# Performance work log

Measured on AMD Instinct MI355X. Metric: run time of the kernel, lower is better.

Reference implementation:

```python
import jax, jax.numpy as jnp
import numpy as np
import math

PHI = (1 + math.sqrt(5)) / 2
ALPHA = 1 / PHI          # residual scale
BETA = 1 / PHI ** 2      # sparse-matmul scale
DIM = 1910
NZ = int(DIM * DIM / PHI)


def setup_inputs() -> dict:
    key = jax.random.key(0)
    kx, ki, kv = jax.random.split(key, 3)
    x = jax.random.normal(kx, (8, 4096, DIM), dtype=jnp.float32)
    W_indices = jax.random.randint(ki, (2, NZ), 0, DIM, dtype=jnp.int32)
    W_values = jax.random.normal(kv, (NZ,), dtype=jnp.float32) / math.sqrt(DIM)
    return {"x": x, "W_indices": W_indices, "W_values": W_values}


def reference(x, W_indices, W_values):
    dim = x.shape[-1]
    # COO -> dense: duplicate (row,col) entries sum, matching torch.sparse semantics.
    W = jnp.zeros((dim, dim), dtype=x.dtype).at[W_indices[0], W_indices[1]].add(W_values)
    orig_shape = x.shape
    xf = x.reshape(-1, dim)          # [tokens, dim]
    Wx = xf @ W.T                    # (W @ x.T).T == x @ W.T
    out = ALPHA * xf + BETA * Wx
    return out.reshape(orig_shape)
```

## Files before the change

### kernel.cpp

```cpp
#include <hip/hip_runtime.h>
#include <hip/hip_bf16.h>
#include <stdint.h>

#define DIMV 1910
#define KP   1920
#define NT   60
#define PHI_F  1.6180339887498949f
#define BETA_F 0.3819660112501051f

typedef __attribute__((ext_vector_type(4))) float f32x4;
typedef __attribute__((ext_vector_type(8))) short bf16x8;
typedef __attribute__((ext_vector_type(8))) unsigned short u16x8;

__device__ __forceinline__ void gl16(const void* g, void* l) {
    __builtin_amdgcn_global_load_lds(
        (const __attribute__((address_space(1))) void*)(uintptr_t)g,
        (__attribute__((address_space(3))) void*)(uint32_t)(uintptr_t)l,
        16, 0, 0);
}

__global__ void k_scatter(const int* __restrict__ ridx, const int* __restrict__ cidx,
                          const float* __restrict__ vals, float* __restrict__ Wd, int nz) {
    int i = blockIdx.x * 256 + threadIdx.x;
    if (i < nz) atomicAdd(Wd + (long)ridx[i] * DIMV + cidx[i], vals[i]);
}

__global__ void k_build_w(const float* __restrict__ Wd, unsigned short* __restrict__ Wb, int total8) {
    int stride = gridDim.x * blockDim.x;
    for (int i = blockIdx.x * blockDim.x + threadIdx.x; i < total8; i += stride) {
        int v = i * 8;
        int n = v / KP;
        int k = v - n * KP;
        u16x8 o;
#pragma unroll
        for (int j = 0; j < 8; ++j) {
            int kk = k + j;
            float fv = (n < DIMV && kk < DIMV) ? Wd[(size_t)n * DIMV + kk] : 0.f;
            if (kk == n && n < DIMV) fv += PHI_F;
            __hip_bfloat16 b = __float2bfloat16(fv);
            o[j] = *reinterpret_cast<unsigned short*>(&b);
        }
        *(u16x8*)(Wb + (size_t)v) = o;
    }
}

__global__ void k_conv_x(const float* __restrict__ x, unsigned short* __restrict__ xb, int total8) {
    int stride = gridDim.x * blockDim.x;
    for (int i = blockIdx.x * blockDim.x + threadIdx.x; i < total8; i += stride) {
        int v = i * 8;
        int row = v / KP;
        int col = v - row * KP;
        u16x8 o;
        if (col + 8 <= DIMV) {
            const float2* s = (const float2*)(x + (size_t)row * DIMV + col);
            float2 f0 = s[0], f1 = s[1], f2 = s[2], f3 = s[3];
            float f[8] = {f0.x, f0.y, f1.x, f1.y, f2.x, f2.y, f3.x, f3.y};
#pragma unroll
            for (int j = 0; j < 8; ++j) {
                __hip_bfloat16 b = __float2bfloat16(f[j]);
                o[j] = *reinterpret_cast<unsigned short*>(&b);
            }
        } else {
#pragma unroll
            for (int j = 0; j < 8; ++j) {
                int c = col + j;
                float fv = (c < DIMV) ? x[(size_t)row * DIMV + c] : 0.f;
                __hip_bfloat16 b = __float2bfloat16(fv);
                o[j] = *reinterpret_cast<unsigned short*>(&b);
            }
        }
        *(u16x8*)(xb + (size_t)v) = o;
    }
}

__global__ __launch_bounds__(512, 2) void k_gemm(const short* __restrict__ A,
                                                 const short* __restrict__ B,
                                                 float* __restrict__ C) {
    __shared__ short As[3 * 256 * 32];
    __shared__ short Bs[3 * 256 * 32];

    const int bid = blockIdx.x;
    const int bn  = bid & 7;
    const int bm  = bid >> 3;

    const int tid = threadIdx.x;
    const int w   = tid >> 6;
    const int l   = tid & 63;
    const int wm  = w >> 2;
    const int wn  = w & 3;
    const int fr  = l & 15;
    const int q   = l >> 4;

    const int srow  = tid >> 2;
    const int lslot = (tid & 3) ^ ((tid >> 3) & 3);
    const char* aG = (const char*)A + ((size_t)(bm * 256 + srow) * KP) * 2 + lslot * 16;
    const char* bG = (const char*)B + ((size_t)(bn * 256 + srow) * KP) * 2 + lslot * 16;
    const size_t gstep = (size_t)128 * KP * 2;
    char* aL0 = (char*)As + tid * 16;
    char* bL0 = (char*)Bs + tid * 16;

    const int co    = (q ^ ((fr >> 1) & 3)) * 16;
    const int aBase = (wm * 128 + fr) * 64 + co;
    const int bBase = (wn * 64  + fr) * 64 + co;

    f32x4 acc[8][4] = {};

#pragma unroll
    for (int tt = 0; tt < 2; ++tt) {
        const char* ga = aG + tt * 64;
        const char* gb = bG + tt * 64;
        char* la = aL0 + tt * 16384;
        char* lb = bL0 + tt * 16384;
        gl16(ga, la); gl16(ga + gstep, la + 8192);
        gl16(gb, lb); gl16(gb + gstep, lb + 8192);
    }
    asm volatile("s_waitcnt vmcnt(4)" ::: "memory");
    __builtin_amdgcn_s_barrier();
    asm volatile("" ::: "memory");

    int rdo = 0;
    int sto = 2 * 16384;

#pragma unroll 3
    for (int t = 0; t < NT; ++t) {
        const char* pa = (const char*)As + rdo + aBase;
        const char* pb = (const char*)Bs + rdo + bBase;

        bf16x8 af[8], b01[2];
#pragma unroll
        for (int mi = 0; mi < 8; ++mi) af[mi] = *(const bf16x8*)(pa + mi * 1024);
#pragma unroll
        for (int ni = 0; ni < 2; ++ni) b01[ni] = *(const bf16x8*)(pb + ni * 1024);
        if (t + 2 < NT) {
            const char* g = aG + (size_t)(t + 2) * 64;
            gl16(g, aL0 + sto); gl16(g + gstep, aL0 + sto + 8192);
        }
        asm volatile("" ::: "memory");
        __builtin_amdgcn_s_barrier();
        asm volatile("" ::: "memory");
        __builtin_amdgcn_s_setprio(1);
#pragma unroll
        for (int mi = 0; mi < 8; ++mi)
#pragma unroll
            for (int ni = 0; ni < 2; ++ni)
                acc[mi][ni] = __builtin_amdgcn_mfma_f32_16x16x32_bf16(af[mi], b01[ni], acc[mi][ni], 0, 0, 0);
        __builtin_amdgcn_s_setprio(0);
        asm volatile("" ::: "memory");
        __builtin_amdgcn_s_barrier();
        asm volatile("" ::: "memory");

        bf16x8 b23[2];
#pragma unroll
        for (int ni = 0; ni < 2; ++ni) b23[ni] = *(const bf16x8*)(pb + (ni + 2) * 1024);
        if (t + 2 < NT) {
            const char* g = bG + (size_t)(t + 2) * 64;
            gl16(g, bL0 + sto); gl16(g + gstep, bL0 + sto + 8192);
            asm volatile("s_waitcnt vmcnt(4)" ::: "memory");
        } else {
            asm volatile("s_waitcnt vmcnt(0)" ::: "memory");
        }
        __builtin_amdgcn_s_barrier();
        asm volatile("" ::: "memory");
        __builtin_amdgcn_s_setprio(1);
#pragma unroll
        for (int mi = 0; mi < 8; ++mi)
#pragma unroll
            for (int ni = 0; ni < 2; ++ni)
                acc[mi][ni + 2] = __builtin_amdgcn_mfma_f32_16x16x32_bf16(af[mi], b23[ni], acc[mi][ni + 2], 0, 0, 0);
        __builtin_amdgcn_s_setprio(0);
        asm volatile("" ::: "memory");
        __builtin_amdgcn_s_barrier();
        asm volatile("" ::: "memory");

        rdo += 16384; if (rdo == 49152) rdo = 0;
        sto += 16384; if (sto == 49152) sto = 0;
    }

    const int grow0 = bm * 256 + wm * 128 + q * 4;
    const int gcol0 = bn * 256 + wn * 64 + fr;
#pragma unroll
    for (int mi = 0; mi < 8; ++mi) {
#pragma unroll
        for (int ni = 0; ni < 4; ++ni) {
            int gcol = gcol0 + ni * 16;
            if (gcol < DIMV) {
                size_t base = (size_t)(grow0 + mi * 16) * DIMV + gcol;
#pragma unroll
                for (int r = 0; r < 4; ++r)
                    C[base + (size_t)r * DIMV] = BETA_F * acc[mi][ni][r];
            }
        }
    }
}

extern "C" void kernel_launch(void* const* d_in, const int* in_sizes, int n_in,
                              void* d_out, int out_size, void* d_ws, size_t ws_size,
                              hipStream_t stream) {
    const float* x    = (const float*)d_in[0];
    const int*   widx = (const int*)d_in[1];
    const float* wval = (const float*)d_in[2];
    float* out = (float*)d_out;

    const int nz = in_sizes[2];
    const int M  = in_sizes[0] / DIMV;

    const size_t xb_bytes = (size_t)M * KP * 2;
    const size_t wb_bytes = (size_t)2048 * KP * 2;
    const size_t wd_bytes = (size_t)DIMV * DIMV * 4;
    char* ws = (char*)d_ws;
    unsigned short* xb = (unsigned short*)ws;
    unsigned short* Wb = (unsigned short*)(ws + xb_bytes);
    float*          Wd = (float*)ws;
    if (ws_size < xb_bytes + wb_bytes) return;
    (void)wd_bytes;

    hipMemsetAsync(Wd, 0, wd_bytes, stream);
    k_scatter<<<(nz + 255) / 256, 256, 0, stream>>>(widx, widx + nz, wval, Wd, nz);
    k_build_w<<<1800, 256, 0, stream>>>(Wd, Wb, KP * KP / 8);
    k_conv_x<<<2048, 256, 0, stream>>>(x, xb, M * KP / 8);
    k_gemm<<<1024, 512, 0, stream>>>((const short*)xb, (const short*)Wb, out);
}
```

Before: 477.2 us.

## Restructure GEMM main loop to K=64 double-buffered tiles with four-phase MFMA schedule

The GEMM K-step grows from 32 to 64, which halves the number of main-loop iterations. The LDS layout changes from a triple buffer of 32-wide tiles to a double buffer of 64-wide tiles (128 KB), using a new XOR swizzle over 8 slots. Each iteration is split into four quadrant phases so LDS fragment loads, global-to-LDS staging and MFMA blocks interleave across barriers. The intent is fewer barriers and less loop overhead per FLOP. The cost is that prefetch depth drops from two stages ahead to one, and the larger LDS footprint may limit occupancy to the declared two blocks per CU.

```diff
diff --git a/kernel.cpp b/kernel.cpp
--- a/kernel.cpp
+++ b/kernel.cpp
@@ -4,7 +4,7 @@
 
 #define DIMV 1910
 #define KP   1920
-#define NT   60
+#define NT   30
 #define PHI_F  1.6180339887498949f
 #define BETA_F 0.3819660112501051f
 
@@ -76,8 +76,7 @@
 __global__ __launch_bounds__(512, 2) void k_gemm(const short* __restrict__ A,
                                                  const short* __restrict__ B,
                                                  float* __restrict__ C) {
-    __shared__ short As[3 * 256 * 32];
-    __shared__ short Bs[3 * 256 * 32];
+    __shared__ char lds[131072];
 
     const int bid = blockIdx.x;
     const int bn  = bid & 7;
@@ -91,90 +90,138 @@
     const int fr  = l & 15;
     const int q   = l >> 4;
 
-    const int srow  = tid >> 2;
-    const int lslot = (tid & 3) ^ ((tid >> 3) & 3);
-    const char* aG = (const char*)A + ((size_t)(bm * 256 + srow) * KP) * 2 + lslot * 16;
-    const char* bG = (const char*)B + ((size_t)(bn * 256 + srow) * KP) * 2 + lslot * 16;
-    const size_t gstep = (size_t)128 * KP * 2;
-    char* aL0 = (char*)As + tid * 16;
-    char* bL0 = (char*)Bs + tid * 16;
-
-    const int co    = (q ^ ((fr >> 1) & 3)) * 16;
-    const int aBase = (wm * 128 + fr) * 64 + co;
-    const int bBase = (wn * 64  + fr) * 64 + co;
+    const int    rs   = tid >> 3;
+    const size_t KPB  = (size_t)KP * 2;
+    const char*  aSrc = (const char*)A + (size_t)(bm * 256 + rs) * KPB + (((tid & 7) ^ (rs & 7)) * 16);
+    const char*  bSrc = (const char*)B + (size_t)(bn * 256 + rs) * KPB + (((tid & 7) ^ (rs & 7)) * 16);
+    char* stDst = lds + tid * 16;
+
+    const int co0  = ((q    ) ^ (fr & 7)) * 16;
+    const int co1  = ((4 + q) ^ (fr & 7)) * 16;
+    const int aOff = (wm * 128 + fr) * 128;
+    const int bOff = 32768 + (wn * 64 + fr) * 128;
 
     f32x4 acc[8][4] = {};
 
-#pragma unroll
-    for (int tt = 0; tt < 2; ++tt) {
-        const char* ga = aG + tt * 64;
-        const char* gb = bG + tt * 64;
-        char* la = aL0 + tt * 16384;
-        char* lb = bL0 + tt * 16384;
-        gl16(ga, la); gl16(ga + gstep, la + 8192);
-        gl16(gb, lb); gl16(gb + gstep, lb + 8192);
-    }
-    asm volatile("s_waitcnt vmcnt(4)" ::: "memory");
+#define STAGE_A(tt, bo, s) gl16(aSrc + (size_t)(s) * 64 * KPB + (size_t)(tt) * 128, stDst + (bo) + (s) * 8192)
+#define STAGE_B(tt, bo, s) gl16(bSrc + (size_t)(s) * 64 * KPB + (size_t)(tt) * 128, stDst + (bo) + 32768 + (s) * 8192)
+
+#pragma unroll
+    for (int s = 0; s < 4; ++s) STAGE_A(0, 0, s);
+#pragma unroll
+    for (int s = 0; s < 4; ++s) STAGE_B(0, 0, s);
+    asm volatile("s_waitcnt vmcnt(0)" ::: "memory");
     __builtin_amdgcn_s_barrier();
     asm volatile("" ::: "memory");
 
-    int rdo = 0;
-    int sto = 2 * 16384;
-
-#pragma unroll 3
+    int bo = 0;
     for (int t = 0; t < NT; ++t) {
-        const char* pa = (const char*)As + rdo + aBase;
-        const char* pb = (const char*)Bs + rdo + bBase;
-
-        bf16x8 af[8], b01[2];
-#pragma unroll
-        for (int mi = 0; mi < 8; ++mi) af[mi] = *(const bf16x8*)(pa + mi * 1024);
-#pragma unroll
-        for (int ni = 0; ni < 2; ++ni) b01[ni] = *(const bf16x8*)(pb + ni * 1024);
-        if (t + 2 < NT) {
-            const char* g = aG + (size_t)(t + 2) * 64;
-            gl16(g, aL0 + sto); gl16(g + gstep, aL0 + sto + 8192);
-        }
-        asm volatile("" ::: "memory");
-        __builtin_amdgcn_s_barrier();
-        asm volatile("" ::: "memory");
-        __builtin_amdgcn_s_setprio(1);
-#pragma unroll
-        for (int mi = 0; mi < 8; ++mi)
-#pragma unroll
-            for (int ni = 0; ni < 2; ++ni)
-                acc[mi][ni] = __builtin_amdgcn_mfma_f32_16x16x32_bf16(af[mi], b01[ni], acc[mi][ni], 0, 0, 0);
-        __builtin_amdgcn_s_setprio(0);
-        asm volatile("" ::: "memory");
-        __builtin_amdgcn_s_barrier();
-        asm volatile("" ::: "memory");
-
-        bf16x8 b23[2];
-#pragma unroll
-        for (int ni = 0; ni < 2; ++ni) b23[ni] = *(const bf16x8*)(pb + (ni + 2) * 1024);
-        if (t + 2 < NT) {
-            const char* g = bG + (size_t)(t + 2) * 64;
-            gl16(g, bL0 + sto); gl16(g + gstep, bL0 + sto + 8192);
-            asm volatile("s_waitcnt vmcnt(4)" ::: "memory");
-        } else {
-            asm volatile("s_waitcnt vmcnt(0)" ::: "memory");
-        }
-        __builtin_amdgcn_s_barrier();
-        asm volatile("" ::: "memory");
-        __builtin_amdgcn_s_setprio(1);
-#pragma unroll
-        for (int mi = 0; mi < 8; ++mi)
-#pragma unroll
-            for (int ni = 0; ni < 2; ++ni)
-                acc[mi][ni + 2] = __builtin_amdgcn_mfma_f32_16x16x32_bf16(af[mi], b23[ni], acc[mi][ni + 2], 0, 0, 0);
-        __builtin_amdgcn_s_setprio(0);
-        asm volatile("" ::: "memory");
-        __builtin_amdgcn_s_barrier();
-        asm volatile("" ::: "memory");
-
-        rdo += 16384; if (rdo == 49152) rdo = 0;
-        sto += 16384; if (sto == 49152) sto = 0;
-    }
+        const int nbo = bo ^ 65536;
+        const char* pa = lds + bo + aOff;
+        const char* pb = lds + bo + bOff;
+        const bool st = (t + 1 < NT);
+        bf16x8 a[4][2], b[2][2];
+
+#pragma unroll
+        for (int mi = 0; mi < 4; ++mi) {
+            a[mi][0] = *(const bf16x8*)(pa + mi * 2048 + co0);
+            a[mi][1] = *(const bf16x8*)(pa + mi * 2048 + co1);
+        }
+#pragma unroll
+        for (int ni = 0; ni < 2; ++ni) {
+            b[ni][0] = *(const bf16x8*)(pb + ni * 2048 + co0);
+            b[ni][1] = *(const bf16x8*)(pb + ni * 2048 + co1);
+        }
+        if (st) { STAGE_A(t + 1, nbo, 0); STAGE_A(t + 1, nbo, 1); STAGE_A(t + 1, nbo, 2); }
+        asm volatile("s_waitcnt lgkmcnt(8)" ::: "memory");
+        __builtin_amdgcn_s_barrier();
+        asm volatile("s_waitcnt lgkmcnt(0)" ::: "memory");
+        __builtin_amdgcn_sched_barrier(0);
+        __builtin_amdgcn_s_setprio(1);
+#pragma unroll
+        for (int kk = 0; kk < 2; ++kk)
+#pragma unroll
+            for (int mi = 0; mi < 4; ++mi)
+#pragma unroll
+                for (int ni = 0; ni < 2; ++ni)
+                    acc[mi][ni] = __builtin_amdgcn_mfma_f32_16x16x32_bf16(a[mi][kk], b[ni][kk], acc[mi][ni], 0, 0, 0);
+        __builtin_amdgcn_s_setprio(0);
+        asm volatile("" ::: "memory");
+        __builtin_amdgcn_s_barrier();
+        asm volatile("" ::: "memory");
+
+#pragma unroll
+        for (int ni = 0; ni < 2; ++ni) {
+            b[ni][0] = *(const bf16x8*)(pb + 4096 + ni * 2048 + co0);
+            b[ni][1] = *(const bf16x8*)(pb + 4096 + ni * 2048 + co1);
+        }
+        if (st) { STAGE_A(t + 1, nbo, 3); STAGE_B(t + 1, nbo, 0); STAGE_B(t + 1, nbo, 1); }
+        asm volatile("" ::: "memory");
+        __builtin_amdgcn_s_barrier();
+        asm volatile("s_waitcnt lgkmcnt(0)" ::: "memory");
+        __builtin_amdgcn_sched_barrier(0);
+        __builtin_amdgcn_s_setprio(1);
+#pragma unroll
+        for (int kk = 0; kk < 2; ++kk)
+#pragma unroll
+            for (int mi = 0; mi < 4; ++mi)
+#pragma unroll
+                for (int ni = 0; ni < 2; ++ni)
+                    acc[mi][ni + 2] = __builtin_amdgcn_mfma_f32_16x16x32_bf16(a[mi][kk], b[ni][kk], acc[mi][ni + 2], 0, 0, 0);
+        __builtin_amdgcn_s_setprio(0);
+        asm volatile("" ::: "memory");
+        __builtin_amdgcn_s_barrier();
+        asm volatile("" ::: "memory");
+
+#pragma unroll
+        for (int mi = 0; mi < 4; ++mi) {
+            a[mi][0] = *(const bf16x8*)(pa + 8192 + mi * 2048 + co0);
+            a[mi][1] = *(const bf16x8*)(pa + 8192 + mi * 2048 + co1);
+        }
+        if (st) { STAGE_B(t + 1, nbo, 2); STAGE_B(t + 1, nbo, 3); }
+        asm volatile("" ::: "memory");
+        __builtin_amdgcn_s_barrier();
+        asm volatile("s_waitcnt lgkmcnt(0)" ::: "memory");
+        __builtin_amdgcn_sched_barrier(0);
+        __builtin_amdgcn_s_setprio(1);
+#pragma unroll
+        for (int kk = 0; kk < 2; ++kk)
+#pragma unroll
+            for (int mi = 0; mi < 4; ++mi)
+#pragma unroll
+                for (int ni = 0; ni < 2; ++ni)
+                    acc[mi + 4][ni + 2] = __builtin_amdgcn_mfma_f32_16x16x32_bf16(a[mi][kk], b[ni][kk], acc[mi + 4][ni + 2], 0, 0, 0);
+        __builtin_amdgcn_s_setprio(0);
+        asm volatile("" ::: "memory");
+        __builtin_amdgcn_s_barrier();
+        asm volatile("" ::: "memory");
+
+#pragma unroll
+        for (int ni = 0; ni < 2; ++ni) {
+            b[ni][0] = *(const bf16x8*)(pb + ni * 2048 + co0);
+            b[ni][1] = *(const bf16x8*)(pb + ni * 2048 + co1);
+        }
+        asm volatile("" ::: "memory");
+        __builtin_amdgcn_s_barrier();
+        asm volatile("s_waitcnt lgkmcnt(0)" ::: "memory");
+        __builtin_amdgcn_sched_barrier(0);
+        __builtin_amdgcn_s_setprio(1);
+#pragma unroll
+        for (int kk = 0; kk < 2; ++kk)
+#pragma unroll
+            for (int mi = 0; mi < 4; ++mi)
+#pragma unroll
+                for (int ni = 0; ni < 2; ++ni)
+                    acc[mi + 4][ni] = __builtin_amdgcn_mfma_f32_16x16x32_bf16(a[mi][kk], b[ni][kk], acc[mi + 4][ni], 0, 0, 0);
+        __builtin_amdgcn_s_setprio(0);
+        asm volatile("s_waitcnt vmcnt(0)" ::: "memory");
+        __builtin_amdgcn_s_barrier();
+        asm volatile("" ::: "memory");
+
+        bo = nbo;
+    }
+#undef STAGE_A
+#undef STAGE_B
 
     const int grow0 = bm * 256 + wm * 128 + q * 4;
     const int gcol0 = bn * 256 + wn * 64 + fr;
```

Result: no change. 473.7 us (-0.7%).
